# Performance work log

Hardware: AMD Instinct MI355X
Metric: run time of the kernel (lower is better)

## Reference

```python
import jax, jax.numpy as jnp
import numpy as np

LAMDA = 0.5
TEMPERATURE = 0.07
EPS = 1e-5


def setup_inputs() -> dict:
    key = jax.random.key(0)
    k1, k2, k3 = jax.random.split(key, 3)
    N, D = 8192, 128
    features = jax.random.normal(k1, (N, D), dtype=jnp.float32)
    labels = jax.random.randint(k2, (N,), 0, 100, dtype=jnp.int64 if jax.config.jax_enable_x64 else jnp.int32)
    domain_labels = jax.random.randint(k3, (N,), 0, 4, dtype=jnp.int64 if jax.config.jax_enable_x64 else jnp.int32)
    return {"features": features, "labels": labels, "domain_labels": domain_labels}


def reference(features, labels, domain_labels):
    N = features.shape[0]
    # L2-normalize rows (torch.nn.functional.normalize, eps=1e-12)
    norms = jnp.maximum(jnp.linalg.norm(features, axis=1, keepdims=True), 1e-12)
    f = features / norms
    sim = jnp.matmul(f, f.T) / TEMPERATURE  # [N, N]

    same_label = labels[:, None] == labels[None, :]
    same_dom = domain_labels[:, None] == domain_labels[None, :]
    offdiag = ~jnp.eye(N, dtype=bool)

    # per-pair domain weight: lamda in-domain, (1-lamda) out-of-domain
    w_exp = jnp.where(same_dom, LAMDA, 1.0 - LAMDA) * jnp.exp(sim)

    # denominator: all off-diagonal pairs (positives + negatives), weighted
    denom = jnp.sum(jnp.where(offdiag, w_exp, 0.0), axis=1) + EPS  # [N]

    pos = same_label & offdiag
    log_frac = jnp.log(w_exp / denom[:, None] + EPS)
    num_pos = jnp.sum(pos, axis=1)  # [N]
    loss_i = jnp.sum(jnp.where(pos, log_frac, 0.0), axis=1) / jnp.maximum(num_pos, 1)

    # anchors with zero positives produce NaN in torch and are skipped
    valid = num_pos > 0
    nans = jnp.sum(~valid)
    loss = -jnp.sum(jnp.where(valid, loss_i, 0.0))
    return loss / (N - nans + 1)
```

## Files before the change

kernel.cpp:

```cpp
#include <hip/hip_runtime.h>

#define NROWS 8192
#define DDIM  128
#define NBLK  (NROWS / 128)
#define NLAB  100
#define GCAP  160
#define GSPL  2
#define GTPB  5
#define EPSV  1e-5f
#define LN2F  0.69314718055994530942f
#define FSCALE 4.53981643f

typedef short s16x8 __attribute__((ext_vector_type(8)));
typedef float f32x4 __attribute__((ext_vector_type(4)));
typedef unsigned short u16;
typedef unsigned int u32;

__device__ __forceinline__ u16 f2bf(float x) {
  u32 b = __builtin_bit_cast(u32, x);
  u32 r = (b + 0x7FFFu + ((b >> 16) & 1u)) >> 16;
  return (u16)r;
}

__global__ __launch_bounds__(256) void norm_kernel(
    const float* __restrict__ feat, u16* __restrict__ g,
    float* __restrict__ denom, float* __restrict__ Lsum,
    int* __restrict__ dcount) {
  int wave = threadIdx.x >> 6;
  int lane = threadIdx.x & 63;
  int row = (blockIdx.x << 2) + wave;
  const float* fr = feat + (size_t)row * DDIM + (lane << 1);
  float2 v = *(const float2*)fr;
  float ss = v.x * v.x + v.y * v.y;
#pragma unroll
  for (int m = 1; m < 64; m <<= 1) ss += __shfl_xor(ss, m);
  float inv = FSCALE / fmaxf(sqrtf(ss), 1e-12f);
  ushort2 o;
  o.x = f2bf(v.x * inv);
  o.y = f2bf(v.y * inv);
  *(ushort2*)(g + (size_t)row * DDIM + (lane << 1)) = o;
  if (lane == 0) denom[row] = 0.0f;
  if (blockIdx.x == 0 && threadIdx.x == 0) { *Lsum = 0.0f; *dcount = 0; }
}

#define LOADB_TO(bv, BsArr, jt)                                              \
  _Pragma("unroll")                                                          \
  for (int kc = 0; kc < 4; ++kc) {                                           \
    const int c_ = (kc << 2) + lh;                                           \
    bv[kc] = *(const s16x8*)(&BsArr[(size_t)((jt)*16 + lr) * DDIM +          \
                                    ((c_ ^ (lr & 7)) << 3)]);                \
  }

#define MFMA_TO(accv, bv, init0, init1)                                      \
  accv[0] = init0; accv[1] = init1;                                          \
  __builtin_amdgcn_s_setprio(1);                                             \
  _Pragma("unroll")                                                          \
  for (int kc = 0; kc < 4; ++kc) {                                           \
    accv[0] = __builtin_amdgcn_mfma_f32_16x16x32_bf16(a[0][kc], bv[kc],      \
                                                      accv[0], 0, 0, 0);     \
    accv[1] = __builtin_amdgcn_mfma_f32_16x16x32_bf16(a[1][kc], bv[kc],      \
                                                      accv[1], 0, 0, 0);     \
  }                                                                          \
  __builtin_amdgcn_s_setprio(0);

#define EPI_T(accv, jt)                                                      \
  {                                                                          \
    const int tj0 = j0 + (jt)*16;                                            \
    float csum = 0.f;                                                        \
    if (diagblk) {                                                           \
      _Pragma("unroll")                                                      \
      for (int rf = 0; rf < 2; ++rf)                                         \
      _Pragma("unroll")                                                      \
        for (int r = 0; r < 4; ++r) {                                        \
          float e_ = __builtin_amdgcn_exp2f(accv[rf][r]);                    \
          e_ = (gibase[rf] + r == tj0 + lr) ? 0.0f : e_;                     \
          dacc[rf][r] += e_;                                                 \
        }                                                                    \
    } else {                                                                 \
      _Pragma("unroll")                                                      \
      for (int rf = 0; rf < 2; ++rf)                                         \
      _Pragma("unroll")                                                      \
        for (int r = 0; r < 4; ++r) {                                        \
          float e_ = __builtin_amdgcn_exp2f(accv[rf][r]);                    \
          dacc[rf][r] += e_;                                                 \
          csum += e_;                                                        \
        }                                                                    \
      csum += __shfl_xor(csum, 16);                                          \
      csum += __shfl_xor(csum, 32);                                          \
      ccol[jt] = csum;                                                       \
    }                                                                        \
  }

__global__ __launch_bounds__(256, 4) void denom_tri(
    const u16* __restrict__ g, float* __restrict__ denom,
    const int* __restrict__ lab, int* __restrict__ offs,
    int* __restrict__ cnts, int* __restrict__ rowlist) {
  const int bi = blockIdx.x, bj = blockIdx.y;
  __shared__ u16 Bs[128 * DDIM];
  const int tid = threadIdx.x;
  if (bj < bi) {
    if (bi == NBLK - 1 && bj == 0) {
      int* h   = (int*)Bs;
      int* cur = h + NLAB;
      int* off = cur + NLAB;
      if (tid < NLAB) h[tid] = 0;
      __syncthreads();
      for (int i = tid; i < NROWS; i += 256) atomicAdd(&h[lab[i]], 1);
      __syncthreads();
      if (tid == 0) {
        int s = 0;
        for (int l = 0; l < NLAB; ++l) { off[l] = s; s += h[l]; }
      }
      __syncthreads();
      if (tid < NLAB) { cur[tid] = off[tid]; offs[tid] = off[tid]; cnts[tid] = h[tid]; }
      __syncthreads();
      for (int i = tid; i < NROWS; i += 256) {
        int p = atomicAdd(&cur[lab[i]], 1);
        rowlist[p] = i;
      }
    }
    return;
  }
  const int wave = tid >> 6, lane = tid & 63;
  const int lr = lane & 15, lh = lane >> 4;
  const int i0 = bi * 128 + wave * 32;
  const int j0 = bj * 128;
  const bool diagblk = (bi == bj);

  {
    const int cs = (tid & 15) ^ ((tid >> 4) & 7);
#pragma unroll
    for (int k = 0; k < 8; ++k) {
      const u16* src = g + (size_t)(j0 + k * 16 + (tid >> 4)) * DDIM + (cs << 3);
      u16* dst = &Bs[(size_t)(k * 16 + (wave << 2)) * DDIM];
      __builtin_amdgcn_global_load_lds(
          (const __attribute__((address_space(1))) void*)src,
          (__attribute__((address_space(3))) void*)dst, 16, 0, 0);
    }
  }

  s16x8 a[2][4];
#pragma unroll
  for (int rf = 0; rf < 2; ++rf) {
    const u16* gr = g + (size_t)(i0 + rf * 16 + lr) * DDIM + lh * 8;
#pragma unroll
    for (int kc = 0; kc < 4; ++kc) a[rf][kc] = *(const s16x8*)(gr + kc * 32);
  }
  const int gibase[2] = {i0 + lh * 4, i0 + 16 + lh * 4};

  asm volatile("s_waitcnt vmcnt(0)" ::: "memory");
  __builtin_amdgcn_s_barrier();

  float dacc[2][4] = {};
  float ccol[8] = {};
  const f32x4 m1 = f32x4{-1.f, -1.f, -1.f, -1.f};

  s16x8 b0[4], b1[4];
  f32x4 acc0[2], acc1[2];

  LOADB_TO(b0, Bs, 0)
  MFMA_TO(acc0, b0, m1, m1)
#pragma unroll
  for (int p = 0; p < 3; ++p) {
    LOADB_TO(b1, Bs, 2 * p + 1)
    MFMA_TO(acc1, b1, m1, m1)
    EPI_T(acc0, 2 * p)
    LOADB_TO(b0, Bs, 2 * p + 2)
    MFMA_TO(acc0, b0, m1, m1)
    EPI_T(acc1, 2 * p + 1)
  }
  LOADB_TO(b1, Bs, 7)
  MFMA_TO(acc1, b1, m1, m1)
  EPI_T(acc0, 6)
  EPI_T(acc1, 7)

#pragma unroll
  for (int rf = 0; rf < 2; ++rf)
#pragma unroll
    for (int r = 0; r < 4; ++r) {
      float v = dacc[rf][r];
      v += __shfl_xor(v, 1); v += __shfl_xor(v, 2);
      v += __shfl_xor(v, 4); v += __shfl_xor(v, 8);
      if (lr == 0) atomicAdd(&denom[gibase[rf] + r], v);
    }
  if (!diagblk) {
#pragma unroll
    for (int jt = 0; jt < 8; ++jt)
      if (lane < 16) atomicAdd(&denom[j0 + jt * 16 + lane], ccol[jt]);
  }
}

__global__ __launch_bounds__(320) void group_loss(
    const u16* __restrict__ g, const int* __restrict__ offs,
    const int* __restrict__ cnts, const int* __restrict__ rowlist,
    const float* __restrict__ denom, float* __restrict__ Lsum,
    int* __restrict__ dcount, float* __restrict__ out) {
  __shared__ u16 Bs[GTPB * 16 * DDIM];
  const int lb = blockIdx.x;
  const int z = blockIdx.y;
  const int cnt = cnts[lb];
  const int off = offs[lb];
  const int tid = threadIdx.x;
  const int wave = tid >> 6, lane = tid & 63;
  const int lr = lane & 15, lh = lane >> 4;
  const bool active = (cnt >= 2) && (z * 16 < cnt);

  if (active) {
#pragma unroll
    for (int s = 0; s < 4; ++s) {
      const int m = s * 320 + tid;
      const int rloc = m >> 4, cc = m & 15;
      const int jt_l = rloc >> 4, rr = rloc & 15;
      const int gidx = (jt_l * GSPL + z) * 16 + rr;
      const int cs = cc ^ (rloc & 7);
      const int grow = rowlist[off + (gidx < cnt ? gidx : 0)];
      const u16* src = g + (size_t)grow * DDIM + (cs << 3);
      u16* dst = &Bs[(size_t)(s * 320 + wave * 64) * 8];
      __builtin_amdgcn_global_load_lds(
          (const __attribute__((address_space(1))) void*)src,
          (__attribute__((address_space(3))) void*)dst, 16, 0, 0);
    }

    s16x8 a[2][4];
#pragma unroll
    for (int rf = 0; rf < 2; ++rf) {
      const int ar = wave * 32 + rf * 16 + lr;
      const int gar = rowlist[off + (ar < cnt ? ar : 0)];
      const u16* gr = g + (size_t)gar * DDIM + lh * 8;
#pragma unroll
      for (int kc = 0; kc < 4; ++kc) a[rf][kc] = *(const s16x8*)(gr + kc * 32);
    }
    const int erow[2] = {wave * 32 + lh * 4, wave * 32 + 16 + lh * 4};
    f32x4 cinit[2];
#pragma unroll
    for (int rf = 0; rf < 2; ++rf)
#pragma unroll
      for (int r = 0; r < 4; ++r) {
        const int er = erow[rf] + r;
        const int gi = rowlist[off + (er < cnt ? er : 0)];
        cinit[rf][r] = -__builtin_amdgcn_logf(denom[gi] + EPSV) - 1.0f;
      }

    asm volatile("s_waitcnt vmcnt(0)" ::: "memory");
    __builtin_amdgcn_s_barrier();

    float lacc[2][4] = {};

#pragma unroll
    for (int jt = 0; jt < GTPB; ++jt) {
      s16x8 b[4];
      LOADB_TO(b, Bs, jt)
      f32x4 acc[2];
      MFMA_TO(acc, b, cinit[0], cinit[1])
      const int col = (jt * GSPL + z) * 16 + lr;
      const bool colok = (col < cnt);
#pragma unroll
      for (int rf = 0; rf < 2; ++rf)
#pragma unroll
        for (int r = 0; r < 4; ++r) {
          const int er = erow[rf] + r;
          const bool valid = colok && (er < cnt) && (er != col);
          float x = __builtin_amdgcn_exp2f(acc[rf][r]) + EPSV;
          float lf = __builtin_amdgcn_logf(x);
          lacc[rf][r] += valid ? lf : 0.0f;
        }
    }

    const float scale = LN2F / (float)(cnt - 1);
    float wtot = 0.f;
#pragma unroll
    for (int rf = 0; rf < 2; ++rf)
#pragma unroll
      for (int r = 0; r < 4; ++r) {
        float v = lacc[rf][r];
        v += __shfl_xor(v, 1); v += __shfl_xor(v, 2);
        v += __shfl_xor(v, 4); v += __shfl_xor(v, 8);
        const int er = erow[rf] + r;
        if (lr == 0 && er < cnt) wtot += v * scale;
      }
    wtot += __shfl_xor(wtot, 1);  wtot += __shfl_xor(wtot, 2);
    wtot += __shfl_xor(wtot, 4);  wtot += __shfl_xor(wtot, 8);
    wtot += __shfl_xor(wtot, 16); wtot += __shfl_xor(wtot, 32);
    if (lane == 0 && wtot != 0.0f) atomicAdd(Lsum, wtot);
  }

  __threadfence();
  __syncthreads();
  if (tid == 0) {
    int done = atomicAdd(dcount, 1);
    if (done == NLAB * GSPL - 1) {
      float L = atomicAdd(Lsum, 0.0f);
      int v = 0;
      for (int l = 0; l < NLAB; ++l) { int c = cnts[l]; v += (c > 1) ? c : 0; }
      out[0] = -L / (float)(v + 1);
    }
  }
}

extern "C" void kernel_launch(void* const* d_in, const int* in_sizes, int n_in,
                              void* d_out, int out_size, void* d_ws, size_t ws_size,
                              hipStream_t stream) {
  const float* feat = (const float*)d_in[0];
  const int* labels = (const int*)d_in[1];
  float* out = (float*)d_out;

  char* ws = (char*)d_ws;
  u16* g        = (u16*)(ws);
  float* denom  = (float*)(ws + (2u << 20));
  int* offs     = (int*)(ws + (2u << 20) + 32768);
  int* cnts     = (int*)(ws + (2u << 20) + 33280);
  float* Lsum   = (float*)(ws + (2u << 20) + 33792);
  int* dcount   = (int*)(ws + (2u << 20) + 33796);
  int* rowlist  = (int*)(ws + (2u << 20) + 65536);

  norm_kernel<<<NROWS / 4, 256, 0, stream>>>(feat, g, denom, Lsum, dcount);
  denom_tri<<<dim3(NBLK, NBLK), 256, 0, stream>>>(g, denom, labels, offs, cnts, rowlist);
  group_loss<<<dim3(NLAB, GSPL), 320, 0, stream>>>(g, offs, cnts, rowlist, denom,
                                                   Lsum, dcount, out);
}
```

Measured before the change: 60.10 us.

## Enlarge denominator tiles to 256 rows per block with four row fragments per wave

The triangular similarity/denominator kernel now gives each block 256 anchor rows against 128 columns, so each wave holds 64 rows (four MFMA row fragments) instead of 32. Each LDS-staged B tile is reused across twice as many rows, and the grid has half as many row-blocks. The diagonal test and the skip condition are adjusted so each unordered pair is still counted once. The cost is a larger A fragment and more accumulators in registers under a 4-waves-per-SIMD launch bound, which may spill or reduce occupancy.

Measured after the change: 92.47 us. 53.9% more time.

```diff
diff --git a/kernel.cpp b/kernel.cpp
--- a/kernel.cpp
+++ b/kernel.cpp
@@ -3,6 +3,7 @@
 #define NROWS 8192
 #define DDIM  128
 #define NBLK  (NROWS / 128)
+#define NBI2  (NBLK / 2)
 #define NLAB  100
 #define GCAP  160
 #define GSPL  2
@@ -50,6 +51,18 @@
     bv[kc] = *(const s16x8*)(&BsArr[(size_t)((jt)*16 + lr) * DDIM +          \
                                     ((c_ ^ (lr & 7)) << 3)]);                \
   }
+
+#define MFMA_TO4(accv, bv, initv)                                            \
+  _Pragma("unroll")                                                          \
+  for (int rf = 0; rf < 4; ++rf) accv[rf] = initv;                           \
+  __builtin_amdgcn_s_setprio(1);                                             \
+  _Pragma("unroll")                                                          \
+  for (int kc = 0; kc < 4; ++kc)                                             \
+    _Pragma("unroll")                                                        \
+    for (int rf = 0; rf < 4; ++rf)                                           \
+      accv[rf] = __builtin_amdgcn_mfma_f32_16x16x32_bf16(a[rf][kc], bv[kc],  \
+                                                         accv[rf], 0, 0, 0);\
+  __builtin_amdgcn_s_setprio(0);
 
 #define MFMA_TO(accv, bv, init0, init1)                                      \
   accv[0] = init0; accv[1] = init1;                                          \
@@ -63,13 +76,12 @@
   }                                                                          \
   __builtin_amdgcn_s_setprio(0);
 
-#define EPI_T(accv, jt)                                                      \
+#define EPI_T4(accv, jt)                                                     \
   {                                                                          \
     const int tj0 = j0 + (jt)*16;                                            \
-    float csum = 0.f;                                                        \
     if (diagblk) {                                                           \
       _Pragma("unroll")                                                      \
-      for (int rf = 0; rf < 2; ++rf)                                         \
+      for (int rf = 0; rf < 4; ++rf)                                         \
       _Pragma("unroll")                                                      \
         for (int r = 0; r < 4; ++r) {                                        \
           float e_ = __builtin_amdgcn_exp2f(accv[rf][r]);                    \
@@ -77,8 +89,9 @@
           dacc[rf][r] += e_;                                                 \
         }                                                                    \
     } else {                                                                 \
+      float csum = 0.f;                                                      \
       _Pragma("unroll")                                                      \
-      for (int rf = 0; rf < 2; ++rf)                                         \
+      for (int rf = 0; rf < 4; ++rf)                                         \
       _Pragma("unroll")                                                      \
         for (int r = 0; r < 4; ++r) {                                        \
           float e_ = __builtin_amdgcn_exp2f(accv[rf][r]);                    \
@@ -98,8 +111,8 @@
   const int bi = blockIdx.x, bj = blockIdx.y;
   __shared__ u16 Bs[128 * DDIM];
   const int tid = threadIdx.x;
-  if (bj < bi) {
-    if (bi == NBLK - 1 && bj == 0) {
+  if (bj < 2 * bi) {
+    if (bi == NBI2 - 1 && bj == 0) {
       int* h   = (int*)Bs;
       int* cur = h + NLAB;
       int* off = cur + NLAB;
@@ -123,9 +136,9 @@
   }
   const int wave = tid >> 6, lane = tid & 63;
   const int lr = lane & 15, lh = lane >> 4;
-  const int i0 = bi * 128 + wave * 32;
+  const int i0 = bi * 256 + wave * 64;
   const int j0 = bj * 128;
-  const bool diagblk = (bi == bj);
+  const bool diagblk = ((bj >> 1) == bi);
 
   {
     const int cs = (tid & 15) ^ ((tid >> 4) & 7);
@@ -139,43 +152,45 @@
     }
   }
 
-  s16x8 a[2][4];
-#pragma unroll
-  for (int rf = 0; rf < 2; ++rf) {
+  s16x8 a[4][4];
+#pragma unroll
+  for (int rf = 0; rf < 4; ++rf) {
     const u16* gr = g + (size_t)(i0 + rf * 16 + lr) * DDIM + lh * 8;
 #pragma unroll
     for (int kc = 0; kc < 4; ++kc) a[rf][kc] = *(const s16x8*)(gr + kc * 32);
   }
-  const int gibase[2] = {i0 + lh * 4, i0 + 16 + lh * 4};
+  int gibase[4];
+#pragma unroll
+  for (int rf = 0; rf < 4; ++rf) gibase[rf] = i0 + rf * 16 + lh * 4;
 
   asm volatile("s_waitcnt vmcnt(0)" ::: "memory");
   __builtin_amdgcn_s_barrier();
 
-  float dacc[2][4] = {};
+  float dacc[4][4] = {};
   float ccol[8] = {};
   const f32x4 m1 = f32x4{-1.f, -1.f, -1.f, -1.f};
 
   s16x8 b0[4], b1[4];
-  f32x4 acc0[2], acc1[2];
+  f32x4 acc0[4], acc1[4];
 
   LOADB_TO(b0, Bs, 0)
-  MFMA_TO(acc0, b0, m1, m1)
+  MFMA_TO4(acc0, b0, m1)
 #pragma unroll
   for (int p = 0; p < 3; ++p) {
     LOADB_TO(b1, Bs, 2 * p + 1)
-    MFMA_TO(acc1, b1, m1, m1)
-    EPI_T(acc0, 2 * p)
+    MFMA_TO4(acc1, b1, m1)
+    EPI_T4(acc0, 2 * p)
     LOADB_TO(b0, Bs, 2 * p + 2)
-    MFMA_TO(acc0, b0, m1, m1)
-    EPI_T(acc1, 2 * p + 1)
+    MFMA_TO4(acc0, b0, m1)
+    EPI_T4(acc1, 2 * p + 1)
   }
   LOADB_TO(b1, Bs, 7)
-  MFMA_TO(acc1, b1, m1, m1)
-  EPI_T(acc0, 6)
-  EPI_T(acc1, 7)
-
-#pragma unroll
-  for (int rf = 0; rf < 2; ++rf)
+  MFMA_TO4(acc1, b1, m1)
+  EPI_T4(acc0, 6)
+  EPI_T4(acc1, 7)
+
+#pragma unroll
+  for (int rf = 0; rf < 4; ++rf)
 #pragma unroll
     for (int r = 0; r < 4; ++r) {
       float v = dacc[rf][r];
@@ -314,7 +329,7 @@
   int* rowlist  = (int*)(ws + (2u << 20) + 65536);
 
   norm_kernel<<<NROWS / 4, 256, 0, stream>>>(feat, g, denom, Lsum, dcount);
-  denom_tri<<<dim3(NBLK, NBLK), 256, 0, stream>>>(g, denom, labels, offs, cnts, rowlist);
+  denom_tri<<<dim3(NBI2, NBLK), 256, 0, stream>>>(g, denom, labels, offs, cnts, rowlist);
   group_loss<<<dim3(NLAB, GSPL), 320, 0, stream>>>(g, offs, cnts, rowlist, denom,
                                                    Lsum, dcount, out);
 }
```
